# Kernel optimization log

Hardware: AMD Instinct MI355X
Metric: run time of the kernel (lower is better)

## Reference

```python
import jax, jax.numpy as jnp
import numpy as np
from math import pi

B = 4096          # batch of frame pairs
W = 4096          # fov_width = pred['f_score'].size(-1)
POS_NUM = 10      # args['fov_pos_num']
NEG_RATIO = 3     # args['fov_neg_ratio']
LAMBDA_FOV = 1.0  # args['lambda']['fov']


def setup_inputs() -> dict:
    key = jax.random.key(0)
    k1, k2, k3, k4 = jax.random.split(key, 4)
    eye = jnp.eye(4, dtype=jnp.float32)
    # near-identity perturbations keep the 3x3 blocks well-conditioned for inverse
    gt_T = eye + 0.3 * jax.random.normal(k1, (B, 4, 4), dtype=jnp.float32)
    gt_e_l = eye + 0.3 * jax.random.normal(k2, (B, 4, 4), dtype=jnp.float32)
    pred_e_l = eye + 0.3 * jax.random.normal(k3, (B, 4, 4), dtype=jnp.float32)
    # BCE input must live strictly in (0,1)
    pred_f_score = jax.random.uniform(k4, (B, W), dtype=jnp.float32,
                                      minval=1e-4, maxval=1.0 - 1e-4)
    return {"gt_sensor2_T_sensor1": gt_T, "gt_e_l": gt_e_l,
            "pred_e_l": pred_e_l, "pred_f_score": pred_f_score}


def _bce(p, y):
    # torch BCELoss clamps each log term at -100
    return -(y * jnp.clip(jnp.log(p), -100.0, None)
             + (1.0 - y) * jnp.clip(jnp.log1p(-p), -100.0, None))


def _gt_fov(axis, fov_width):
    # axis: [B,3] = (f_l_inv @ e1), i.e. first column of f_l_inv
    yaw = jnp.arctan2(axis[:, 1], axis[:, 0])                 # [B]
    f_idx = (-yaw + pi) / (2.0 * pi) * fov_width              # in [0, W]
    xmin = f_idx.astype(jnp.int32) - POS_NUM // 2             # int() truncation == floor for f_idx>=0
    cols = jnp.arange(fov_width)
    # all three branches of the torch loop are a wraparound window of POS_NUM ones
    return (((cols[None, :] - xmin[:, None]) % fov_width) < POS_NUM).astype(jnp.float32)


def reference(gt_sensor2_T_sensor1, gt_e_l, pred_e_l, pred_f_score):
    Rinv = jnp.linalg.inv(gt_sensor2_T_sensor1[:, :3, :3])    # [B,3,3]

    # gt_f_axis = bmm(pred_e_l @ Rinv, e1) -> first column
    f_l_inv_pred = jnp.einsum('bij,bjk->bik', pred_e_l[:, :3, :3], Rinv)
    gt_f_score = _gt_fov(f_l_inv_pred[:, :, 0], pred_f_score.shape[-1])  # [B,W]

    # gt['f_l'] = 4x4 embed of inverse(gt_e_l @ Rinv)
    f_l_inv_gt = jnp.einsum('bij,bjk->bik', gt_e_l[:, :3, :3], Rinv)
    R33 = jnp.linalg.inv(f_l_inv_gt)
    f_l = jnp.tile(jnp.eye(4, dtype=jnp.float32), (gt_f_score.shape[0], 1, 1))
    f_l = f_l.at[:, :3, :3].set(R33)

    # SSD-style hard negative mining over the fov bins
    bce = _bce(pred_f_score, gt_f_score)                      # [B,W]
    pos = gt_f_score > 0
    loss_c = jnp.where(pos, 0.0, bce)
    order = jnp.argsort(-loss_c, axis=1)                      # descending sort indices
    rank = jnp.argsort(order, axis=1)                         # rank of each bin
    num_pos = pos.sum(axis=1, keepdims=True)
    num_neg = jnp.minimum(NEG_RATIO * num_pos, pos.shape[1] - 1)
    neg = rank < num_neg
    weighted = jnp.logical_or(pos, neg)
    wf = weighted.astype(pred_f_score.dtype)
    # torch gathers an equal count per row then takes the mean -> masked mean
    loss_fov = jnp.sum(bce * wf) / jnp.sum(wf)
    return loss_fov * LAMBDA_FOV, gt_f_score, f_l
```

## Files before the change

### kernel.cpp

```cpp
#include <hip/hip_runtime.h>
#include <math.h>

#define BATCH 4096
#define W 4096
#define POS_NUM 10
#define NUM_NEG 30
#define SEL_PER_ROW 40
#define TPB 256

__device__ __forceinline__ void inv3x3(const double* m, double* inv) {
  double a = m[0], b = m[1], c = m[2], d = m[3], e = m[4], f = m[5],
         g = m[6], h = m[7], i = m[8];
  double A = e * i - f * h, B = f * g - d * i, C = d * h - e * g;
  double det = a * A + b * B + c * C;
  double id = 1.0 / det;
  inv[0] = A * id; inv[1] = (c * h - b * i) * id; inv[2] = (b * f - c * e) * id;
  inv[3] = B * id; inv[4] = (a * i - c * g) * id; inv[5] = (c * d - a * f) * id;
  inv[6] = C * id; inv[7] = (b * g - a * h) * id; inv[8] = (a * e - b * d) * id;
}

__global__ __launch_bounds__(TPB) void row_kernel(
    const float* __restrict__ gt_T, const float* __restrict__ gt_e,
    const float* __restrict__ pred_e, const float* __restrict__ pred,
    float* __restrict__ gt_out, float* __restrict__ fl_out,
    float* __restrict__ row_sum) {
  int b = blockIdx.x;
  int tid = threadIdx.x;
  __shared__ float cand[W];
  __shared__ unsigned s_cnt;
  __shared__ int s_xmin;
  __shared__ float s_pos[TPB / 64];
  if (tid == 0) s_cnt = 0;

  const float4* prow = (const float4*)(pred + (size_t)b * W);
  float4 pv[4];
  #pragma unroll
  for (int k = 0; k < 4; ++k) pv[k] = prow[tid + k * TPB];

  if (tid == 0) {
    const float* T = gt_T + (size_t)b * 16;
    const float* E = gt_e + (size_t)b * 16;
    const float* P = pred_e + (size_t)b * 16;
    double r[9], e[9], p[9];
    #pragma unroll
    for (int i = 0; i < 3; ++i)
      #pragma unroll
      for (int j = 0; j < 3; ++j) {
        r[i * 3 + j] = (double)T[i * 4 + j];
        e[i * 3 + j] = (double)E[i * 4 + j];
        p[i * 3 + j] = (double)P[i * 4 + j];
      }
    double rinv[9];
    inv3x3(r, rinv);
    double ax = p[0] * rinv[0] + p[1] * rinv[3] + p[2] * rinv[6];
    double ay = p[3] * rinv[0] + p[4] * rinv[3] + p[5] * rinv[6];
    double yaw = atan2(ay, ax);
    double fidx = (-yaw + M_PI) / (2.0 * M_PI) * (double)W;
    s_xmin = (int)fidx - POS_NUM / 2;

    double m[9];
    #pragma unroll
    for (int i = 0; i < 3; ++i)
      #pragma unroll
      for (int j = 0; j < 3; ++j)
        m[i * 3 + j] = e[i * 3 + 0] * rinv[0 * 3 + j] +
                       e[i * 3 + 1] * rinv[1 * 3 + j] +
                       e[i * 3 + 2] * rinv[2 * 3 + j];
    double R[9];
    inv3x3(m, R);
    float* fl = fl_out + (size_t)b * 16;
    fl[0] = (float)R[0]; fl[1] = (float)R[1]; fl[2]  = (float)R[2]; fl[3]  = 0.f;
    fl[4] = (float)R[3]; fl[5] = (float)R[4]; fl[6]  = (float)R[5]; fl[7]  = 0.f;
    fl[8] = (float)R[6]; fl[9] = (float)R[7]; fl[10] = (float)R[8]; fl[11] = 0.f;
    fl[12] = 0.f; fl[13] = 0.f; fl[14] = 0.f; fl[15] = 1.f;
  }
  __syncthreads();
  int xmin = s_xmin;

  float4* grow = (float4*)(gt_out + (size_t)b * W);
  float pp[16];
  float pos_sum = 0.f;
  #pragma unroll
  for (int k = 0; k < 4; ++k) {
    int w0 = (tid + k * TPB) * 4;
    pp[k * 4 + 0] = pv[k].x; pp[k * 4 + 1] = pv[k].y;
    pp[k * 4 + 2] = pv[k].z; pp[k * 4 + 3] = pv[k].w;
    float4 g;
    float* gc = (float*)&g;
    #pragma unroll
    for (int j = 0; j < 4; ++j) {
      bool q = (((w0 + j - xmin) & (W - 1)) < POS_NUM);
      gc[j] = q ? 1.f : 0.f;
      if (q) {
        pos_sum += fminf(-logf(pp[k * 4 + j]), 100.f);
        pp[k * 4 + j] = -3.f;
      }
    }
    grow[tid + k * TPB] = g;
  }

  float thi = 1e30f;
  float tlo = 0.9865f;
  while (true) {
    int loc = 0;
    #pragma unroll
    for (int j = 0; j < 16; ++j) loc += ((pp[j] > tlo) && (pp[j] <= thi)) ? 1 : 0;
    if (loc) {
      unsigned base = atomicAdd(&s_cnt, (unsigned)loc);
      #pragma unroll
      for (int j = 0; j < 16; ++j)
        if ((pp[j] > tlo) && (pp[j] <= thi)) cand[base++] = pp[j];
    }
    __syncthreads();
    if (s_cnt >= NUM_NEG || tlo <= -0.5f) break;
    thi = tlo;
    tlo = (tlo > 0.9f) ? 0.9f : -1.0f;
    __syncthreads();
  }

  float s = pos_sum;
  #pragma unroll
  for (int off = 32; off >= 1; off >>= 1) s += __shfl_xor(s, off);
  if ((tid & 63) == 0) s_pos[tid >> 6] = s;
  __syncthreads();

  if (tid < 64) {
    unsigned C = s_cnt;
    float tsum = 0.f;
    for (unsigned base0 = 0; base0 < C; base0 += 64) {
      unsigned myi = base0 + (unsigned)tid;
      bool valid = (myi < C);
      float mine = valid ? cand[myi] : -1.f;
      int rank = valid ? 0 : NUM_NEG;
      for (unsigned j = 0; j < C; ++j) {
        float cj = cand[j];
        rank += ((cj > mine) || (cj == mine && j < myi)) ? 1 : 0;
      }
      if (rank < NUM_NEG) tsum += fminf(-log1pf(-mine), 100.f);
    }
    #pragma unroll
    for (int off = 32; off >= 1; off >>= 1) tsum += __shfl_xor(tsum, off);
    if (tid == 0)
      row_sum[b] = tsum + s_pos[0] + s_pos[1] + s_pos[2] + s_pos[3];
  }
}

__global__ __launch_bounds__(TPB) void reduce_kernel(
    const float* __restrict__ row_sum, float* __restrict__ out) {
  int tid = threadIdx.x;
  double acc = 0.0;
  for (int i = tid; i < BATCH; i += TPB) acc += (double)row_sum[i];
  #pragma unroll
  for (int off = 32; off >= 1; off >>= 1) acc += __shfl_xor(acc, off);
  __shared__ double sh[4];
  int wid = tid >> 6, lane = tid & 63;
  if (lane == 0) sh[wid] = acc;
  __syncthreads();
  if (tid == 0) {
    double total = sh[0] + sh[1] + sh[2] + sh[3];
    out[0] = (float)(total / (double)((size_t)SEL_PER_ROW * BATCH));
  }
}

extern "C" void kernel_launch(void* const* d_in, const int* in_sizes, int n_in,
                              void* d_out, int out_size, void* d_ws, size_t ws_size,
                              hipStream_t stream) {
  const float* gt_T   = (const float*)d_in[0];
  const float* gt_e   = (const float*)d_in[1];
  const float* pred_e = (const float*)d_in[2];
  const float* pred_f = (const float*)d_in[3];
  float* out = (float*)d_out;
  float* gt_score = out + 1;
  float* fl = out + 1 + (size_t)BATCH * W;
  float* row_sum = (float*)d_ws;

  row_kernel<<<BATCH, TPB, 0, stream>>>(gt_T, gt_e, pred_e, pred_f,
                                        gt_score, fl, row_sum);
  reduce_kernel<<<1, TPB, 0, stream>>>(row_sum, out);
}
```

Baseline: 132.8 us.

## Split per-row kernel into matrix, streaming, and top-k stages with global candidate buffers

```diff
diff --git a/kernel.cpp b/kernel.cpp
--- a/kernel.cpp
+++ b/kernel.cpp
@@ -7,6 +7,10 @@
 #define NUM_NEG 30
 #define SEL_PER_ROW 40
 #define TPB 256
+#define CAP 256
+#define CAND_TH 0.98f
+
+typedef float f4 __attribute__((ext_vector_type(4)));
 
 __device__ __forceinline__ void inv3x3(const double* m, double* inv) {
   double a = m[0], b = m[1], c = m[2], d = m[3], e = m[4], f = m[5],
@@ -19,130 +23,147 @@
   inv[6] = C * id; inv[7] = (b * g - a * h) * id; inv[8] = (a * e - b * d) * id;
 }
 
-__global__ __launch_bounds__(TPB) void row_kernel(
+__global__ __launch_bounds__(TPB) void mat_kernel(
     const float* __restrict__ gt_T, const float* __restrict__ gt_e,
-    const float* __restrict__ pred_e, const float* __restrict__ pred,
-    float* __restrict__ gt_out, float* __restrict__ fl_out,
-    float* __restrict__ row_sum) {
-  int b = blockIdx.x;
-  int tid = threadIdx.x;
-  __shared__ float cand[W];
-  __shared__ unsigned s_cnt;
-  __shared__ int s_xmin;
-  __shared__ float s_pos[TPB / 64];
-  if (tid == 0) s_cnt = 0;
-
-  const float4* prow = (const float4*)(pred + (size_t)b * W);
-  float4 pv[4];
-  #pragma unroll
-  for (int k = 0; k < 4; ++k) pv[k] = prow[tid + k * TPB];
-
-  if (tid == 0) {
-    const float* T = gt_T + (size_t)b * 16;
-    const float* E = gt_e + (size_t)b * 16;
-    const float* P = pred_e + (size_t)b * 16;
-    double r[9], e[9], p[9];
-    #pragma unroll
-    for (int i = 0; i < 3; ++i)
+    const float* __restrict__ pred_e, int* __restrict__ xmin_out,
+    float* __restrict__ fl_out, int* __restrict__ cnt,
+    float* __restrict__ pos_row) {
+  int b = blockIdx.x * TPB + threadIdx.x;
+  if (b >= BATCH) return;
+  cnt[b] = 0;
+  pos_row[b] = 0.f;
+  const float* T = gt_T + (size_t)b * 16;
+  const float* E = gt_e + (size_t)b * 16;
+  const float* P = pred_e + (size_t)b * 16;
+  double r[9], e[9], p[9];
+  #pragma unroll
+  for (int i = 0; i < 3; ++i)
+    #pragma unroll
+    for (int j = 0; j < 3; ++j) {
+      r[i * 3 + j] = (double)T[i * 4 + j];
+      e[i * 3 + j] = (double)E[i * 4 + j];
+      p[i * 3 + j] = (double)P[i * 4 + j];
+    }
+  double rinv[9];
+  inv3x3(r, rinv);
+  double ax = p[0] * rinv[0] + p[1] * rinv[3] + p[2] * rinv[6];
+  double ay = p[3] * rinv[0] + p[4] * rinv[3] + p[5] * rinv[6];
+  double yaw = atan2(ay, ax);
+  double fidx = (-yaw + M_PI) / (2.0 * M_PI) * (double)W;
+  xmin_out[b] = (int)fidx - POS_NUM / 2;
+
+  double m[9];
+  #pragma unroll
+  for (int i = 0; i < 3; ++i)
+    #pragma unroll
+    for (int j = 0; j < 3; ++j)
+      m[i * 3 + j] = e[i * 3 + 0] * rinv[0 * 3 + j] +
+                     e[i * 3 + 1] * rinv[1 * 3 + j] +
+                     e[i * 3 + 2] * rinv[2 * 3 + j];
+  double R[9];
+  inv3x3(m, R);
+  float* fl = fl_out + (size_t)b * 16;
+  fl[0] = (float)R[0]; fl[1] = (float)R[1]; fl[2]  = (float)R[2]; fl[3]  = 0.f;
+  fl[4] = (float)R[3]; fl[5] = (float)R[4]; fl[6]  = (float)R[5]; fl[7]  = 0.f;
+  fl[8] = (float)R[6]; fl[9] = (float)R[7]; fl[10] = (float)R[8]; fl[11] = 0.f;
+  fl[12] = 0.f; fl[13] = 0.f; fl[14] = 0.f; fl[15] = 1.f;
+}
+
+#define SBLK 2048
+#define SIT 8
+__global__ __launch_bounds__(TPB) void stream_kernel(
+    const float* __restrict__ pred, const int* __restrict__ xmin_arr,
+    float* __restrict__ gt_out, int* __restrict__ cnt,
+    float* __restrict__ pos_row, float* __restrict__ candv) {
+  int g0 = blockIdx.x * TPB + threadIdx.x;
+  const int STRIDE = SBLK * TPB;
+  #pragma unroll
+  for (int it = 0; it < SIT; ++it) {
+    int g = g0 + it * STRIDE;
+    int row = g >> 10;
+    int c4 = g & 1023;
+    int xm = xmin_arr[row];
+    f4 pv = ((const f4*)pred)[g];
+    int off0 = ((c4 << 2) - xm) & (W - 1);
+    float psum = 0.f;
+    bool anyp = false;
+    bool cd[4];
+    int loc = 0;
+    f4 gt;
+    #pragma unroll
+    for (int j = 0; j < 4; ++j) {
+      bool pos = (((off0 + j) & (W - 1)) < POS_NUM);
+      gt[j] = pos ? 1.f : 0.f;
+      cd[j] = (!pos) && (pv[j] > CAND_TH);
+      loc += cd[j] ? 1 : 0;
+      if (pos) { psum += fminf(-logf(pv[j]), 100.f); anyp = true; }
+    }
+    __builtin_nontemporal_store(gt, (f4*)gt_out + g);
+    if (anyp) atomicAdd(&pos_row[row], psum);
+    if (loc) {
+      int base = atomicAdd(&cnt[row], loc);
       #pragma unroll
-      for (int j = 0; j < 3; ++j) {
-        r[i * 3 + j] = (double)T[i * 4 + j];
-        e[i * 3 + j] = (double)E[i * 4 + j];
-        p[i * 3 + j] = (double)P[i * 4 + j];
-      }
-    double rinv[9];
-    inv3x3(r, rinv);
-    double ax = p[0] * rinv[0] + p[1] * rinv[3] + p[2] * rinv[6];
-    double ay = p[3] * rinv[0] + p[4] * rinv[3] + p[5] * rinv[6];
-    double yaw = atan2(ay, ax);
-    double fidx = (-yaw + M_PI) / (2.0 * M_PI) * (double)W;
-    s_xmin = (int)fidx - POS_NUM / 2;
-
-    double m[9];
-    #pragma unroll
-    for (int i = 0; i < 3; ++i)
-      #pragma unroll
-      for (int j = 0; j < 3; ++j)
-        m[i * 3 + j] = e[i * 3 + 0] * rinv[0 * 3 + j] +
-                       e[i * 3 + 1] * rinv[1 * 3 + j] +
-                       e[i * 3 + 2] * rinv[2 * 3 + j];
-    double R[9];
-    inv3x3(m, R);
-    float* fl = fl_out + (size_t)b * 16;
-    fl[0] = (float)R[0]; fl[1] = (float)R[1]; fl[2]  = (float)R[2]; fl[3]  = 0.f;
-    fl[4] = (float)R[3]; fl[5] = (float)R[4]; fl[6]  = (float)R[5]; fl[7]  = 0.f;
-    fl[8] = (float)R[6]; fl[9] = (float)R[7]; fl[10] = (float)R[8]; fl[11] = 0.f;
-    fl[12] = 0.f; fl[13] = 0.f; fl[14] = 0.f; fl[15] = 1.f;
+      for (int j = 0; j < 4; ++j)
+        if (cd[j]) { if (base < CAP) candv[(size_t)row * CAP + base] = pv[j]; ++base; }
+    }
   }
-  __syncthreads();
-  int xmin = s_xmin;
-
-  float4* grow = (float4*)(gt_out + (size_t)b * W);
-  float pp[16];
-  float pos_sum = 0.f;
-  #pragma unroll
-  for (int k = 0; k < 4; ++k) {
-    int w0 = (tid + k * TPB) * 4;
-    pp[k * 4 + 0] = pv[k].x; pp[k * 4 + 1] = pv[k].y;
-    pp[k * 4 + 2] = pv[k].z; pp[k * 4 + 3] = pv[k].w;
-    float4 g;
-    float* gc = (float*)&g;
-    #pragma unroll
-    for (int j = 0; j < 4; ++j) {
-      bool q = (((w0 + j - xmin) & (W - 1)) < POS_NUM);
-      gc[j] = q ? 1.f : 0.f;
-      if (q) {
-        pos_sum += fminf(-logf(pp[k * 4 + j]), 100.f);
-        pp[k * 4 + j] = -3.f;
-      }
-    }
-    grow[tid + k * TPB] = g;
-  }
-
-  float thi = 1e30f;
-  float tlo = 0.9865f;
-  while (true) {
-    int loc = 0;
-    #pragma unroll
-    for (int j = 0; j < 16; ++j) loc += ((pp[j] > tlo) && (pp[j] <= thi)) ? 1 : 0;
-    if (loc) {
-      unsigned base = atomicAdd(&s_cnt, (unsigned)loc);
-      #pragma unroll
-      for (int j = 0; j < 16; ++j)
-        if ((pp[j] > tlo) && (pp[j] <= thi)) cand[base++] = pp[j];
-    }
-    __syncthreads();
-    if (s_cnt >= NUM_NEG || tlo <= -0.5f) break;
-    thi = tlo;
-    tlo = (tlo > 0.9f) ? 0.9f : -1.0f;
-    __syncthreads();
-  }
-
-  float s = pos_sum;
-  #pragma unroll
-  for (int off = 32; off >= 1; off >>= 1) s += __shfl_xor(s, off);
-  if ((tid & 63) == 0) s_pos[tid >> 6] = s;
-  __syncthreads();
-
-  if (tid < 64) {
-    unsigned C = s_cnt;
-    float tsum = 0.f;
-    for (unsigned base0 = 0; base0 < C; base0 += 64) {
-      unsigned myi = base0 + (unsigned)tid;
+}
+
+__global__ __launch_bounds__(64) void topk_kernel(
+    const float* __restrict__ pred, const int* __restrict__ xmin_arr,
+    const int* __restrict__ cnt, const float* __restrict__ pos_row,
+    const float* __restrict__ candv, float* __restrict__ row_sum) {
+  int r = blockIdx.x;
+  int lane = threadIdx.x;
+  __shared__ float vals[W];
+  int C = cnt[r];
+  float tsum = 0.f;
+  if (C >= NUM_NEG && C <= CAP) {
+    const float* cv = candv + (size_t)r * CAP;
+    for (int base = 0; base < C; base += 64) {
+      int myi = base + lane;
       bool valid = (myi < C);
-      float mine = valid ? cand[myi] : -1.f;
+      float mine = valid ? cv[myi] : -1.f;
       int rank = valid ? 0 : NUM_NEG;
-      for (unsigned j = 0; j < C; ++j) {
-        float cj = cand[j];
+      for (int j = 0; j < C; ++j) {
+        float cj = cv[j];
         rank += ((cj > mine) || (cj == mine && j < myi)) ? 1 : 0;
       }
       if (rank < NUM_NEG) tsum += fminf(-log1pf(-mine), 100.f);
     }
     #pragma unroll
     for (int off = 32; off >= 1; off >>= 1) tsum += __shfl_xor(tsum, off);
-    if (tid == 0)
-      row_sum[b] = tsum + s_pos[0] + s_pos[1] + s_pos[2] + s_pos[3];
+  } else {
+    int xm = xmin_arr[r];
+    const float* prow = pred + (size_t)r * W;
+    for (int k = 0; k < W / 64; ++k) {
+      int w = lane + k * 64;
+      bool pos = (((w - xm) & (W - 1)) < POS_NUM);
+      vals[w] = pos ? -1.f : prow[w];
+    }
+    __syncthreads();
+    float t = 1e30f;
+    int taken = 0;
+    while (taken < NUM_NEG) {
+      float lm = -1.f;
+      for (int k = 0; k < W / 64; ++k) {
+        float v = vals[lane + k * 64];
+        if (v < t) lm = fmaxf(lm, v);
+      }
+      #pragma unroll
+      for (int off = 32; off >= 1; off >>= 1) lm = fmaxf(lm, __shfl_xor(lm, off));
+      if (lm < 0.f) break;
+      int lc = 0;
+      for (int k = 0; k < W / 64; ++k) lc += (vals[lane + k * 64] == lm) ? 1 : 0;
+      #pragma unroll
+      for (int off = 32; off >= 1; off >>= 1) lc += __shfl_xor(lc, off);
+      int k2 = min(lc, NUM_NEG - taken);
+      tsum += (float)k2 * fminf(-log1pf(-lm), 100.f);
+      taken += k2;
+      t = lm;
+    }
   }
+  if (lane == 0) row_sum[r] = tsum + pos_row[r];
 }
 
 __global__ __launch_bounds__(TPB) void reduce_kernel(
@@ -172,9 +193,18 @@
   float* out = (float*)d_out;
   float* gt_score = out + 1;
   float* fl = out + 1 + (size_t)BATCH * W;
-  float* row_sum = (float*)d_ws;
-
-  row_kernel<<<BATCH, TPB, 0, stream>>>(gt_T, gt_e, pred_e, pred_f,
-                                        gt_score, fl, row_sum);
+
+  int*   xmin_ws = (int*)d_ws;
+  int*   cnt     = xmin_ws + BATCH;
+  float* pos_row = (float*)(cnt + BATCH);
+  float* row_sum = pos_row + BATCH;
+  float* candv   = row_sum + BATCH;
+
+  mat_kernel<<<BATCH / TPB, TPB, 0, stream>>>(gt_T, gt_e, pred_e, xmin_ws, fl,
+                                              cnt, pos_row);
+  stream_kernel<<<SBLK, TPB, 0, stream>>>(pred_f, xmin_ws, gt_score, cnt,
+                                          pos_row, candv);
+  topk_kernel<<<BATCH, 64, 0, stream>>>(pred_f, xmin_ws, cnt, pos_row, candv,
+                                        row_sum);
   reduce_kernel<<<1, TPB, 0, stream>>>(row_sum, out);
 }
```

Result: slower. 232.4 us (+75.0%).

## Split matrix math into separate kernel and single-pass candidate selection with fallback

Applied to the files above, without the earlier changes.

```diff
diff --git a/kernel.cpp b/kernel.cpp
--- a/kernel.cpp
+++ b/kernel.cpp
@@ -7,6 +7,10 @@
 #define NUM_NEG 30
 #define SEL_PER_ROW 40
 #define TPB 256
+#define CAP 256
+#define CAND_TH 0.985f
+
+typedef float f4 __attribute__((ext_vector_type(4)));
 
 __device__ __forceinline__ void inv3x3(const double* m, double* inv) {
   double a = m[0], b = m[1], c = m[2], d = m[3], e = m[4], f = m[5],
@@ -19,129 +23,152 @@
   inv[6] = C * id; inv[7] = (b * g - a * h) * id; inv[8] = (a * e - b * d) * id;
 }
 
+__global__ __launch_bounds__(TPB) void mat_kernel(
+    const float* __restrict__ gt_T, const float* __restrict__ gt_e,
+    const float* __restrict__ pred_e, int* __restrict__ xmin_out,
+    float* __restrict__ fl_out) {
+  int b = blockIdx.x * TPB + threadIdx.x;
+  if (b >= BATCH) return;
+  const float* T = gt_T + (size_t)b * 16;
+  const float* E = gt_e + (size_t)b * 16;
+  const float* P = pred_e + (size_t)b * 16;
+  double r[9], e[9], p[9];
+  #pragma unroll
+  for (int i = 0; i < 3; ++i)
+    #pragma unroll
+    for (int j = 0; j < 3; ++j) {
+      r[i * 3 + j] = (double)T[i * 4 + j];
+      e[i * 3 + j] = (double)E[i * 4 + j];
+      p[i * 3 + j] = (double)P[i * 4 + j];
+    }
+  double rinv[9];
+  inv3x3(r, rinv);
+  double ax = p[0] * rinv[0] + p[1] * rinv[3] + p[2] * rinv[6];
+  double ay = p[3] * rinv[0] + p[4] * rinv[3] + p[5] * rinv[6];
+  double yaw = atan2(ay, ax);
+  double fidx = (-yaw + M_PI) / (2.0 * M_PI) * (double)W;
+  xmin_out[b] = (int)fidx - POS_NUM / 2;
+
+  double m[9];
+  #pragma unroll
+  for (int i = 0; i < 3; ++i)
+    #pragma unroll
+    for (int j = 0; j < 3; ++j)
+      m[i * 3 + j] = e[i * 3 + 0] * rinv[0 * 3 + j] +
+                     e[i * 3 + 1] * rinv[1 * 3 + j] +
+                     e[i * 3 + 2] * rinv[2 * 3 + j];
+  double R[9];
+  inv3x3(m, R);
+  float* fl = fl_out + (size_t)b * 16;
+  fl[0] = (float)R[0]; fl[1] = (float)R[1]; fl[2]  = (float)R[2]; fl[3]  = 0.f;
+  fl[4] = (float)R[3]; fl[5] = (float)R[4]; fl[6]  = (float)R[5]; fl[7]  = 0.f;
+  fl[8] = (float)R[6]; fl[9] = (float)R[7]; fl[10] = (float)R[8]; fl[11] = 0.f;
+  fl[12] = 0.f; fl[13] = 0.f; fl[14] = 0.f; fl[15] = 1.f;
+}
+
 __global__ __launch_bounds__(TPB) void row_kernel(
-    const float* __restrict__ gt_T, const float* __restrict__ gt_e,
-    const float* __restrict__ pred_e, const float* __restrict__ pred,
-    float* __restrict__ gt_out, float* __restrict__ fl_out,
-    float* __restrict__ row_sum) {
+    const float* __restrict__ pred, const int* __restrict__ xmin_arr,
+    float* __restrict__ gt_out, float* __restrict__ row_sum) {
   int b = blockIdx.x;
   int tid = threadIdx.x;
-  __shared__ float cand[W];
+  __shared__ float cand[CAP];
   __shared__ unsigned s_cnt;
-  __shared__ int s_xmin;
-  __shared__ float s_pos[TPB / 64];
+  __shared__ float s_red[TPB / 64];
   if (tid == 0) s_cnt = 0;
-
-  const float4* prow = (const float4*)(pred + (size_t)b * W);
-  float4 pv[4];
+  int xmin = xmin_arr[b];
+
+  const f4* prow = (const f4*)(pred + (size_t)b * W);
+  f4 pv[4];
   #pragma unroll
   for (int k = 0; k < 4; ++k) pv[k] = prow[tid + k * TPB];
 
-  if (tid == 0) {
-    const float* T = gt_T + (size_t)b * 16;
-    const float* E = gt_e + (size_t)b * 16;
-    const float* P = pred_e + (size_t)b * 16;
-    double r[9], e[9], p[9];
-    #pragma unroll
-    for (int i = 0; i < 3; ++i)
-      #pragma unroll
-      for (int j = 0; j < 3; ++j) {
-        r[i * 3 + j] = (double)T[i * 4 + j];
-        e[i * 3 + j] = (double)E[i * 4 + j];
-        p[i * 3 + j] = (double)P[i * 4 + j];
-      }
-    double rinv[9];
-    inv3x3(r, rinv);
-    double ax = p[0] * rinv[0] + p[1] * rinv[3] + p[2] * rinv[6];
-    double ay = p[3] * rinv[0] + p[4] * rinv[3] + p[5] * rinv[6];
-    double yaw = atan2(ay, ax);
-    double fidx = (-yaw + M_PI) / (2.0 * M_PI) * (double)W;
-    s_xmin = (int)fidx - POS_NUM / 2;
-
-    double m[9];
-    #pragma unroll
-    for (int i = 0; i < 3; ++i)
-      #pragma unroll
-      for (int j = 0; j < 3; ++j)
-        m[i * 3 + j] = e[i * 3 + 0] * rinv[0 * 3 + j] +
-                       e[i * 3 + 1] * rinv[1 * 3 + j] +
-                       e[i * 3 + 2] * rinv[2 * 3 + j];
-    double R[9];
-    inv3x3(m, R);
-    float* fl = fl_out + (size_t)b * 16;
-    fl[0] = (float)R[0]; fl[1] = (float)R[1]; fl[2]  = (float)R[2]; fl[3]  = 0.f;
-    fl[4] = (float)R[3]; fl[5] = (float)R[4]; fl[6]  = (float)R[5]; fl[7]  = 0.f;
-    fl[8] = (float)R[6]; fl[9] = (float)R[7]; fl[10] = (float)R[8]; fl[11] = 0.f;
-    fl[12] = 0.f; fl[13] = 0.f; fl[14] = 0.f; fl[15] = 1.f;
-  }
   __syncthreads();
-  int xmin = s_xmin;
-
-  float4* grow = (float4*)(gt_out + (size_t)b * W);
+
+  f4* grow = (f4*)(gt_out + (size_t)b * W);
   float pp[16];
   float pos_sum = 0.f;
   #pragma unroll
   for (int k = 0; k < 4; ++k) {
     int w0 = (tid + k * TPB) * 4;
-    pp[k * 4 + 0] = pv[k].x; pp[k * 4 + 1] = pv[k].y;
-    pp[k * 4 + 2] = pv[k].z; pp[k * 4 + 3] = pv[k].w;
-    float4 g;
-    float* gc = (float*)&g;
+    f4 gt;
     #pragma unroll
     for (int j = 0; j < 4; ++j) {
+      float p = pv[k][j];
       bool q = (((w0 + j - xmin) & (W - 1)) < POS_NUM);
-      gc[j] = q ? 1.f : 0.f;
-      if (q) {
-        pos_sum += fminf(-logf(pp[k * 4 + j]), 100.f);
-        pp[k * 4 + j] = -3.f;
+      gt[j] = q ? 1.f : 0.f;
+      if (q) { pos_sum += fminf(-logf(p), 100.f); p = -3.f; }
+      pp[k * 4 + j] = p;
+    }
+    __builtin_nontemporal_store(gt, grow + (tid + k * TPB));
+  }
+
+  int loc = 0;
+  #pragma unroll
+  for (int j = 0; j < 16; ++j) loc += (pp[j] > CAND_TH) ? 1 : 0;
+  if (loc) {
+    unsigned base = atomicAdd(&s_cnt, (unsigned)loc);
+    #pragma unroll
+    for (int j = 0; j < 16; ++j)
+      if (pp[j] > CAND_TH) { if (base < CAP) cand[base] = pp[j]; ++base; }
+  }
+
+  float s = pos_sum;
+  #pragma unroll
+  for (int off = 32; off >= 1; off >>= 1) s += __shfl_xor(s, off);
+  if ((tid & 63) == 0) s_red[tid >> 6] = s;
+  __syncthreads();
+  unsigned C = s_cnt;
+  float posT = s_red[0] + s_red[1] + s_red[2] + s_red[3];
+
+  if (C >= NUM_NEG && C <= CAP) {
+    if (tid < 64) {
+      float tsum = 0.f;
+      for (unsigned base0 = 0; base0 < C; base0 += 64) {
+        unsigned myi = base0 + (unsigned)tid;
+        bool valid = (myi < C);
+        float mine = valid ? cand[myi] : -1.f;
+        int rank = valid ? 0 : NUM_NEG;
+        for (unsigned j = 0; j < C; ++j) {
+          float cj = cand[j];
+          rank += ((cj > mine) || (cj == mine && j < myi)) ? 1 : 0;
+        }
+        if (rank < NUM_NEG) tsum += fminf(-log1pf(-mine), 100.f);
       }
-    }
-    grow[tid + k * TPB] = g;
-  }
-
-  float thi = 1e30f;
-  float tlo = 0.9865f;
-  while (true) {
-    int loc = 0;
-    #pragma unroll
-    for (int j = 0; j < 16; ++j) loc += ((pp[j] > tlo) && (pp[j] <= thi)) ? 1 : 0;
-    if (loc) {
-      unsigned base = atomicAdd(&s_cnt, (unsigned)loc);
+      #pragma unroll
+      for (int off = 32; off >= 1; off >>= 1) tsum += __shfl_xor(tsum, off);
+      if (tid == 0) row_sum[b] = tsum + posT;
+    }
+  } else {
+    float t = 2.f;
+    int taken = 0;
+    float acc = 0.f;
+    while (taken < NUM_NEG) {
+      float lm = -1.f;
       #pragma unroll
       for (int j = 0; j < 16; ++j)
-        if ((pp[j] > tlo) && (pp[j] <= thi)) cand[base++] = pp[j];
-    }
-    __syncthreads();
-    if (s_cnt >= NUM_NEG || tlo <= -0.5f) break;
-    thi = tlo;
-    tlo = (tlo > 0.9f) ? 0.9f : -1.0f;
-    __syncthreads();
-  }
-
-  float s = pos_sum;
-  #pragma unroll
-  for (int off = 32; off >= 1; off >>= 1) s += __shfl_xor(s, off);
-  if ((tid & 63) == 0) s_pos[tid >> 6] = s;
-  __syncthreads();
-
-  if (tid < 64) {
-    unsigned C = s_cnt;
-    float tsum = 0.f;
-    for (unsigned base0 = 0; base0 < C; base0 += 64) {
-      unsigned myi = base0 + (unsigned)tid;
-      bool valid = (myi < C);
-      float mine = valid ? cand[myi] : -1.f;
-      int rank = valid ? 0 : NUM_NEG;
-      for (unsigned j = 0; j < C; ++j) {
-        float cj = cand[j];
-        rank += ((cj > mine) || (cj == mine && j < myi)) ? 1 : 0;
-      }
-      if (rank < NUM_NEG) tsum += fminf(-log1pf(-mine), 100.f);
-    }
-    #pragma unroll
-    for (int off = 32; off >= 1; off >>= 1) tsum += __shfl_xor(tsum, off);
-    if (tid == 0)
-      row_sum[b] = tsum + s_pos[0] + s_pos[1] + s_pos[2] + s_pos[3];
+        if (pp[j] < t) lm = fmaxf(lm, pp[j]);
+      #pragma unroll
+      for (int off = 32; off >= 1; off >>= 1) lm = fmaxf(lm, __shfl_xor(lm, off));
+      if ((tid & 63) == 0) s_red[tid >> 6] = lm;
+      __syncthreads();
+      float bm = fmaxf(fmaxf(s_red[0], s_red[1]), fmaxf(s_red[2], s_red[3]));
+      __syncthreads();
+      if (bm < 0.f) break;
+      int lc = 0;
+      #pragma unroll
+      for (int j = 0; j < 16; ++j) lc += (pp[j] == bm) ? 1 : 0;
+      #pragma unroll
+      for (int off = 32; off >= 1; off >>= 1) lc += __shfl_xor(lc, off);
+      if ((tid & 63) == 0) s_red[tid >> 6] = (float)lc;
+      __syncthreads();
+      int bc = (int)(s_red[0] + s_red[1] + s_red[2] + s_red[3]);
+      __syncthreads();
+      int k2 = min(bc, NUM_NEG - taken);
+      acc += (float)k2 * fminf(-log1pf(-bm), 100.f);
+      taken += k2;
+      t = bm;
+    }
+    if (tid == 0) row_sum[b] = acc + posT;
   }
 }
 
@@ -172,9 +199,11 @@
   float* out = (float*)d_out;
   float* gt_score = out + 1;
   float* fl = out + 1 + (size_t)BATCH * W;
-  float* row_sum = (float*)d_ws;
-
-  row_kernel<<<BATCH, TPB, 0, stream>>>(gt_T, gt_e, pred_e, pred_f,
-                                        gt_score, fl, row_sum);
+
+  int*   xmin_ws = (int*)d_ws;
+  float* row_sum = (float*)(xmin_ws + BATCH);
+
+  mat_kernel<<<BATCH / TPB, TPB, 0, stream>>>(gt_T, gt_e, pred_e, xmin_ws, fl);
+  row_kernel<<<BATCH, TPB, 0, stream>>>(pred_f, xmin_ws, gt_score, row_sum);
   reduce_kernel<<<1, TPB, 0, stream>>>(row_sum, out);
 }
```

New measurement: 129.9 us. 2.1% less time.
